# Kernel optimization log

Measured on AMD Instinct MI355X. Metric: run time of the kernel, lower is better.

## Reference

```python
import jax, jax.numpy as jnp
import numpy as np

N, D0, D1, HID, OUT = 4096, 256, 128, 64, 16
R, M, K, PROJ = 3, 2, 2, 128  # meta-path rels, same-type rels, schema rels, attn hidden


def setup_inputs() -> dict:
    key = jax.random.key(0)
    ks = jax.random.split(key, 24)
    g = lambda i, shape, s: jax.random.normal(ks[i], shape, jnp.float32) * s
    return {
        "features0": g(0, (N, D0), 1.0),
        "features1": g(1, (N, D1), 1.0),
        # row-scale adjacencies so aggregated features stay O(1)
        "adj_same": jax.random.uniform(ks[2], (M, N, N), jnp.float32) / N,
        "adj_meta": jax.random.uniform(ks[3], (R, N, N), jnp.float32) / N,
        "adj_schema": jax.random.uniform(ks[4], (K, N, N), jnp.float32) / N,
        "Wm0": g(5, (D0, HID), D0 ** -0.5), "bm0": jnp.zeros((HID,), jnp.float32),
        "Wm1": g(6, (D1, HID), D1 ** -0.5), "bm1": jnp.zeros((HID,), jnp.float32),
        "Wa": g(7, (HID, PROJ), HID ** -0.5), "ba": jnp.zeros((PROJ,), jnp.float32),
        "qa": g(8, (PROJ,), PROJ ** -0.5),
        "ws": g(9, (HID, 1), HID ** -0.5),
        "Wc1": g(10, (HID, PROJ), HID ** -0.5), "bc1": jnp.zeros((PROJ,), jnp.float32),
        "wc2": g(11, (PROJ, 1), PROJ ** -0.5),
        "Wt1": g(12, (HID, PROJ), HID ** -0.5), "bt1": jnp.zeros((PROJ,), jnp.float32),
        "wt2": g(13, (PROJ, 1), PROJ ** -0.5),
        "Wp": g(14, (HID, OUT), HID ** -0.5), "bp": jnp.zeros((OUT,), jnp.float32),
    }


def reference(features0, features1, adj_same, adj_meta, adj_schema,
              Wm0, bm0, Wm1, bm1, Wa, ba, qa, ws, Wc1, bc1, wc2,
              Wt1, bt1, wt2, Wp, bp):
    # per-type feature mapping: tanh(Linear(x))
    h0 = jnp.tanh(features0 @ Wm0 + bm0)  # [N, HID]
    h1 = jnp.tanh(features1 @ Wm1 + bm1)  # [N, HID]

    # --- Dif_Classes_AGG: meta-path aggregation + semantic attention over R relations ---
    hr = jnp.tanh(jnp.einsum('rij,jd->rid', adj_meta, h0))        # [R, N, HID]
    s = jnp.mean(jnp.tanh(hr @ Wa + ba) @ qa, axis=1)             # [R]
    beta_r = jax.nn.softmax(s)                                    # [R]
    relation_agg = jnp.einsum('r,rnd->nd', beta_r, hr)            # [N, HID]

    # --- Weight_Schema: schema-matrix aggregation with per-node softmax over K ---
    zk = jnp.einsum('kij,jd->kid', adj_schema, h1)                # [K, N, HID]
    beta_k = jax.nn.softmax(jnp.squeeze(zk @ ws, -1), axis=0)     # [K, N]
    item_classes_agg = jnp.einsum('kn,knd->nd', beta_k, zk)       # [N, HID]

    # --- Classes_Relation_AGG: same-type (item-item) aggregation over M relations ---
    ym = jnp.tanh(jnp.einsum('mij,jd->mid', adj_same, item_classes_agg))  # [M, N, HID]
    wm = jnp.squeeze(jnp.tanh(ym @ Wc1 + bc1) @ wc2, -1)          # [M, N]
    beta_m = jax.nn.softmax(wm, axis=0)                           # [M, N]
    item_item = jnp.einsum('mn,mnd->nd', beta_m, ym)              # [N, HID]

    # --- AggAttention over the two module outputs ---
    Hs = jnp.stack([relation_agg, item_item], axis=1)             # [N, 2, HID]
    wt = jnp.squeeze(jnp.tanh(Hs @ Wt1 + bt1) @ wt2, -1)          # [N, 2]
    beta_t = jax.nn.softmax(wt, axis=1)[..., None]                # [N, 2, 1]
    H = jnp.sum(beta_t * Hs, axis=1)                              # [N, HID]

    return (H @ Wp + bp, H)
```

## Files before the change

### kernel.cpp

```cpp
#include <hip/hip_runtime.h>

#define NODES 4096

typedef float f32x4 __attribute__((ext_vector_type(4)));
typedef float f32x8 __attribute__((ext_vector_type(8)));
typedef __bf16 bf16x8 __attribute__((ext_vector_type(8)));
typedef unsigned short u16x8 __attribute__((ext_vector_type(8)));

__device__ __forceinline__ unsigned short f2bf(float x) {
    unsigned u = __builtin_bit_cast(unsigned, x);
    return (unsigned short)((u + 0x7fffu + ((u >> 16) & 1u)) >> 16);
}

__device__ __forceinline__ void glds16(const void* g, void* l) {
    __builtin_amdgcn_global_load_lds(
        (const __attribute__((address_space(1))) unsigned int*)g,
        (__attribute__((address_space(3))) unsigned int*)l,
        16, 0, 0);
}

__global__ __launch_bounds__(256) void prep_h(
    const float* __restrict__ f0, const float* __restrict__ f1,
    const float* __restrict__ Wm0, const float* __restrict__ bm0,
    const float* __restrict__ Wm1, const float* __restrict__ bm1,
    unsigned short* __restrict__ hT0, unsigned short* __restrict__ hT1)
{
    const int d = threadIdx.x & 63;
    int n = blockIdx.x * 4 + (threadIdx.x >> 6);
    n = __builtin_amdgcn_readfirstlane(n);
    const float* r0 = f0 + (size_t)n * 256;
    float a0 = bm0[d];
#pragma unroll 8
    for (int k = 0; k < 256; ++k) a0 = fmaf(r0[k], Wm0[k * 64 + d], a0);
    hT0[(size_t)d * NODES + n] = f2bf(tanhf(a0));
    const float* r1 = f1 + (size_t)n * 128;
    float a1 = bm1[d];
#pragma unroll 8
    for (int k = 0; k < 128; ++k) a1 = fmaf(r1[k], Wm1[k * 64 + d], a1);
    hT1[(size_t)d * NODES + n] = f2bf(tanhf(a1));
}

__global__ __launch_bounds__(256, 2) void adj_gemm(
    const float* __restrict__ A0, const float* __restrict__ A1,
    const float* __restrict__ A2, const float* __restrict__ A3,
    const float* __restrict__ A4,
    const unsigned short* __restrict__ hTa, const unsigned short* __restrict__ hTb,
    int split, float* __restrict__ outBase, unsigned tanhMask,
    int khBits, int klen)
{
    __shared__ unsigned short sB[2][64][256];

    const int job = blockIdx.y;
    const float* adj = job == 0 ? A0 : job == 1 ? A1 : job == 2 ? A2 : job == 3 ? A3 : A4;
    const unsigned short* hT = (job < split) ? hTa : hTb;
    const bool doTanh = (tanhMask >> job) & 1u;

    const int bx = blockIdx.x;
    const int group = bx >> khBits;
    const int kh = bx & ((1 << khBits) - 1);
    const int kc0 = kh * klen;
    const int nchunks = klen >> 8;
    const int n0 = group * 64;

    const int lane = threadIdx.x & 63;
    const int wid = threadIdx.x >> 6;
    const int fr = lane & 15, fg = lane >> 4;

    const char* hB = (const char*)hT;
    char* ldsBase = (char*)&sB[0][0][0];

    const int gd_half = lane >> 5;
    const int gd_kb = (lane & 31) * 16;

    const char* aPtr = (const char*)adj +
        ((size_t)(n0 + wid * 16 + fr) * NODES + kc0 + fg * 8) * 4;

    f32x4 acc0 = {0.f,0.f,0.f,0.f}, acc1 = {0.f,0.f,0.f,0.f};
    f32x4 acc2 = {0.f,0.f,0.f,0.f}, acc3 = {0.f,0.f,0.f,0.f};

    {
        const size_t cbyte = (size_t)kc0 * 2;
#pragma unroll
        for (int i = 0; i < 8; ++i) {
            const int seg = wid * 8 + i;
            char* ldst = ldsBase + seg * 1024;
            const int d = seg * 2 + gd_half;
            const int sb = gd_kb ^ ((d & 7) << 4);
            glds16(hB + (size_t)d * (NODES * 2) + cbyte + sb, ldst);
        }
    }
    __syncthreads();

    int cur = 0;
    for (int c = 0; c < nchunks; ++c) {
        if (c + 1 < nchunks) {
            const size_t cbyte = (size_t)(kc0 + ((c + 1) << 8)) * 2;
            const int bufoff = (cur ^ 1) * 32768;
#pragma unroll
            for (int i = 0; i < 8; ++i) {
                const int seg = wid * 8 + i;
                char* ldst = ldsBase + bufoff + seg * 1024;
                const int d = seg * 2 + gd_half;
                const int sb = gd_kb ^ ((d & 7) << 4);
                glds16(hB + (size_t)d * (NODES * 2) + cbyte + sb, ldst);
            }
        }
        const char* bb = ldsBase + cur * 32768;
        const char* aC = aPtr + ((size_t)c << 10);
#pragma unroll
        for (int ks = 0; ks < 8; ++ks) {
            f32x8 av = *(const f32x8*)(aC + (ks << 7));
            bf16x8 af = __builtin_convertvector(av, bf16x8);
            {
                const int dcol = 0 * 16 + fr;
                const int off = dcol * 512 + (((ks << 6) + (fg << 4)) ^ ((dcol & 7) << 4));
                u16x8 bf = *(const u16x8*)(bb + off);
                acc0 = __builtin_amdgcn_mfma_f32_16x16x32_bf16(af, __builtin_bit_cast(bf16x8, bf), acc0, 0, 0, 0);
            }
            {
                const int dcol = 1 * 16 + fr;
                const int off = dcol * 512 + (((ks << 6) + (fg << 4)) ^ ((dcol & 7) << 4));
                u16x8 bf = *(const u16x8*)(bb + off);
                acc1 = __builtin_amdgcn_mfma_f32_16x16x32_bf16(af, __builtin_bit_cast(bf16x8, bf), acc1, 0, 0, 0);
            }
            {
                const int dcol = 2 * 16 + fr;
                const int off = dcol * 512 + (((ks << 6) + (fg << 4)) ^ ((dcol & 7) << 4));
                u16x8 bf = *(const u16x8*)(bb + off);
                acc2 = __builtin_amdgcn_mfma_f32_16x16x32_bf16(af, __builtin_bit_cast(bf16x8, bf), acc2, 0, 0, 0);
            }
            {
                const int dcol = 3 * 16 + fr;
                const int off = dcol * 512 + (((ks << 6) + (fg << 4)) ^ ((dcol & 7) << 4));
                u16x8 bf = *(const u16x8*)(bb + off);
                acc3 = __builtin_amdgcn_mfma_f32_16x16x32_bf16(af, __builtin_bit_cast(bf16x8, bf), acc3, 0, 0, 0);
            }
        }
        __syncthreads();
        cur ^= 1;
    }

    float* outC = outBase + (size_t)((job << khBits) | kh) * (NODES * 64);
    float* Cw = outC + (size_t)(n0 + wid * 16 + fg * 4) * 64 + fr;
#pragma unroll
    for (int j = 0; j < 4; ++j) {
        float v0 = acc0[j], v1 = acc1[j], v2 = acc2[j], v3 = acc3[j];
        if (doTanh) { v0 = tanhf(v0); v1 = tanhf(v1); v2 = tanhf(v2); v3 = tanhf(v3); }
        Cw[(size_t)j * 64 + 0]  = v0; Cw[(size_t)j * 64 + 16] = v1;
        Cw[(size_t)j * 64 + 32] = v2; Cw[(size_t)j * 64 + 48] = v3;
    }
}

__global__ __launch_bounds__(128) void stage_c(
    const float* __restrict__ agg, const float* __restrict__ Wa,
    const float* __restrict__ ba, const float* __restrict__ qa,
    const float* __restrict__ wsv, float* __restrict__ sacc,
    unsigned short* __restrict__ iccT)
{
    const int n = blockIdx.x;
    const int p = threadIdx.x;
    __shared__ float rs[3][2];
    __shared__ float ru[2][2];

    const float* h0p = agg + (size_t)n * 64;
    const float* h1p = agg + ((size_t)NODES + n) * 64;
    const float* h2p = agg + ((size_t)2 * NODES + n) * 64;
    float a0 = ba[p], a1 = a0, a2 = a0;
#pragma unroll 8
    for (int d = 0; d < 64; ++d) {
        float w = Wa[d * 128 + p];
        a0 = fmaf(h0p[d], w, a0);
        a1 = fmaf(h1p[d], w, a1);
        a2 = fmaf(h2p[d], w, a2);
    }
    float qv = qa[p];
    float v0 = tanhf(a0) * qv, v1 = tanhf(a1) * qv, v2 = tanhf(a2) * qv;

    const float* z0 = agg + ((size_t)3 * NODES + n) * 64;
    const float* z1 = agg + ((size_t)4 * NODES + n) * 64;
    float u0 = (p < 64) ? z0[p] * wsv[p] : 0.f;
    float u1 = (p < 64) ? z1[p] * wsv[p] : 0.f;

#pragma unroll
    for (int off = 32; off; off >>= 1) {
        v0 += __shfl_down(v0, off); v1 += __shfl_down(v1, off); v2 += __shfl_down(v2, off);
        u0 += __shfl_down(u0, off); u1 += __shfl_down(u1, off);
    }
    if ((p & 63) == 0) {
        int w = p >> 6;
        rs[0][w] = v0; rs[1][w] = v1; rs[2][w] = v2;
        ru[0][w] = u0; ru[1][w] = u1;
    }
    __syncthreads();
    if (p < 3) atomicAdd(&sacc[p], rs[p][0] + rs[p][1]);

    float U0 = ru[0][0] + ru[0][1];
    float U1 = ru[1][0] + ru[1][1];
    float mx = fmaxf(U0, U1);
    float e0 = expf(U0 - mx), e1 = expf(U1 - mx);
    float inv = 1.f / (e0 + e1);
    if (p < 64) {
        float icc = (e0 * z0[p] + e1 * z1[p]) * inv;
        iccT[(size_t)p * NODES + n] = f2bf(icc);
    }
}

__global__ __launch_bounds__(256) void finalize(
    const float* __restrict__ agg, const float* __restrict__ ymp,
    const float* __restrict__ sacc,
    const float* __restrict__ Wc1, const float* __restrict__ bc1, const float* __restrict__ wc2,
    const float* __restrict__ Wt1, const float* __restrict__ bt1, const float* __restrict__ wt2,
    const float* __restrict__ Wp, const float* __restrict__ bp,
    float* __restrict__ out)
{
    __shared__ float sWc[64 * 128];
    __shared__ float sWp[64 * 16];
    __shared__ float sY0[2][64], sY1[2][64];
    __shared__ float sHs0[2][64], sHs1[2][64], sHv[2][64];
    __shared__ float rA[2][2], rB[2][2];

    const int t = threadIdx.x;
    for (int i = t; i < 64 * 128; i += 256) sWc[i] = Wc1[i];
    for (int i = t; i < 64 * 16; i += 256) sWp[i] = Wp[i];

    float s0 = sacc[0] * (1.f / NODES), s1 = sacc[1] * (1.f / NODES), s2 = sacc[2] * (1.f / NODES);
    float sm = fmaxf(s0, fmaxf(s1, s2));
    float b0 = expf(s0 - sm), b1 = expf(s1 - sm), b2 = expf(s2 - sm);
    float bi = 1.f / (b0 + b1 + b2);
    b0 *= bi; b1 *= bi; b2 *= bi;

    const int sub = t >> 7;
    const int p = t & 127;
    const int wiH = p >> 6;
    const float bcv = bc1[p], wcv = wc2[p], btv = bt1[p], wtv = wt2[p];
    __syncthreads();

    for (int it = 0; it < 8; ++it) {
        const int n = blockIdx.x * 16 + it * 2 + sub;
        if (p < 64) {
            const size_t NN64 = (size_t)NODES * 64;
            float ya = ymp[(size_t)n * 64 + p]            + ymp[NN64 + (size_t)n * 64 + p];
            float yb = ymp[2 * NN64 + (size_t)n * 64 + p] + ymp[3 * NN64 + (size_t)n * 64 + p];
            sY0[sub][p] = tanhf(ya);
            sY1[sub][p] = tanhf(yb);
            sHs0[sub][p] = b0 * agg[(size_t)n * 64 + p]
                         + b1 * agg[((size_t)NODES + n) * 64 + p]
                         + b2 * agg[((size_t)2 * NODES + n) * 64 + p];
        }
        __syncthreads();
        float ac0 = bcv, ac1 = bcv;
#pragma unroll 8
        for (int d = 0; d < 64; ++d) {
            float w = sWc[d * 128 + p];
            ac0 = fmaf(sY0[sub][d], w, ac0);
            ac1 = fmaf(sY1[sub][d], w, ac1);
        }
        float v0 = tanhf(ac0) * wcv, v1 = tanhf(ac1) * wcv;
#pragma unroll
        for (int off = 32; off; off >>= 1) { v0 += __shfl_down(v0, off); v1 += __shfl_down(v1, off); }
        if ((p & 63) == 0) { rA[sub][wiH] = v0; rB[sub][wiH] = v1; }
        __syncthreads();
        float wm0 = rA[sub][0] + rA[sub][1];
        float wm1 = rB[sub][0] + rB[sub][1];
        float mm = fmaxf(wm0, wm1);
        float g0 = expf(wm0 - mm), g1 = expf(wm1 - mm);
        float gi = 1.f / (g0 + g1);
        g0 *= gi; g1 *= gi;
        if (p < 64) sHs1[sub][p] = g0 * sY0[sub][p] + g1 * sY1[sub][p];
        __syncthreads();

        float at0 = btv, at1 = btv;
#pragma unroll 8
        for (int d = 0; d < 64; ++d) {
            float w = Wt1[d * 128 + p];
            at0 = fmaf(sHs0[sub][d], w, at0);
            at1 = fmaf(sHs1[sub][d], w, at1);
        }
        float q0 = tanhf(at0) * wtv, q1 = tanhf(at1) * wtv;
#pragma unroll
        for (int off = 32; off; off >>= 1) { q0 += __shfl_down(q0, off); q1 += __shfl_down(q1, off); }
        if ((p & 63) == 0) { rA[sub][wiH] = q0; rB[sub][wiH] = q1; }
        __syncthreads();
        float t0 = rA[sub][0] + rA[sub][1];
        float t1 = rB[sub][0] + rB[sub][1];
        float tm = fmaxf(t0, t1);
        float c0 = expf(t0 - tm), c1 = expf(t1 - tm);
        float ci = 1.f / (c0 + c1);
        c0 *= ci; c1 *= ci;
        if (p < 64) {
            float H = c0 * sHs0[sub][p] + c1 * sHs1[sub][p];
            sHv[sub][p] = H;
            out[(size_t)NODES * 16 + (size_t)n * 64 + p] = H;
        }
        __syncthreads();
        if (p < 16) {
            float a = bp[p];
#pragma unroll 8
            for (int d = 0; d < 64; ++d) a = fmaf(sHv[sub][d], sWp[d * 16 + p], a);
            out[(size_t)n * 16 + p] = a;
        }
        __syncthreads();
    }
}

extern "C" void kernel_launch(void* const* d_in, const int* in_sizes, int n_in,
                              void* d_out, int out_size, void* d_ws, size_t ws_size,
                              hipStream_t stream)
{
    const float* f0   = (const float*)d_in[0];
    const float* f1   = (const float*)d_in[1];
    const float* adjS = (const float*)d_in[2];
    const float* adjM = (const float*)d_in[3];
    const float* adjK = (const float*)d_in[4];
    const float* Wm0  = (const float*)d_in[5];
    const float* bm0  = (const float*)d_in[6];
    const float* Wm1  = (const float*)d_in[7];
    const float* bm1  = (const float*)d_in[8];
    const float* Wa   = (const float*)d_in[9];
    const float* ba   = (const float*)d_in[10];
    const float* qa   = (const float*)d_in[11];
    const float* wsv  = (const float*)d_in[12];
    const float* Wc1  = (const float*)d_in[13];
    const float* bc1  = (const float*)d_in[14];
    const float* wc2  = (const float*)d_in[15];
    const float* Wt1  = (const float*)d_in[16];
    const float* bt1  = (const float*)d_in[17];
    const float* wt2  = (const float*)d_in[18];
    const float* Wp   = (const float*)d_in[19];
    const float* bpv  = (const float*)d_in[20];
    float* out = (float*)d_out;

    char* ws = (char*)d_ws;
    unsigned short* hT0  = (unsigned short*)(ws);
    unsigned short* hT1  = (unsigned short*)(ws + 524288);
    unsigned short* iccT = (unsigned short*)(ws + 1048576);
    float* agg           = (float*)(ws + 1572864);
    float* ymp           = (float*)(ws + 4718592);
    float* sacc          = (float*)(ws + 8912896);

    hipMemsetAsync(sacc, 0, 64, stream);
    prep_h<<<dim3(1024), dim3(256), 0, stream>>>(f0, f1, Wm0, bm0, Wm1, bm1, hT0, hT1);

    const size_t NNs = (size_t)NODES * NODES;
    adj_gemm<<<dim3(64, 5), dim3(256), 0, stream>>>(
        adjM, adjM + NNs, adjM + 2 * NNs, adjK, adjK + NNs,
        hT0, hT1, 3, agg, 0x7u, 0, 4096);
    stage_c<<<dim3(4096), dim3(128), 0, stream>>>(agg, Wa, ba, qa, wsv, sacc, iccT);
    adj_gemm<<<dim3(128, 2), dim3(256), 0, stream>>>(
        adjS, adjS + NNs, adjS, adjS, adjS,
        iccT, iccT, 5, ymp, 0x0u, 1, 2048);
    finalize<<<dim3(256), dim3(256), 0, stream>>>(
        agg, ymp, sacc, Wc1, bc1, wc2, Wt1, bt1, wt2, Wp, bpv, out);
}
```

Baseline: 299.1 us.

## Stream adjacency tiles through LDS with async loads alongside bf16 h tiles

The adjacency GEMM previously read fp32 adjacency rows directly from global memory into registers while only the h operand was staged in LDS. Now both the adjacency tile and the h tile are fetched with global_load_lds into a double-buffered 96KB LDS region using XOR swizzles. Prefetch runs two chunks ahead, with explicit vmcnt waits and raw barriers. The chunk size is halved to 128 columns and the occupancy hint is dropped. The aim is to hide HBM latency of the dominant fp32 adjacency stream, at the cost of more LDS (likely one block per CU) and hand-tuned waitcnt correctness.

Measured after the change: 256.1 us. 1.17x faster.

```diff
diff --git a/kernel.cpp b/kernel.cpp
--- a/kernel.cpp
+++ b/kernel.cpp
@@ -40,7 +40,7 @@
     hT1[(size_t)d * NODES + n] = f2bf(tanhf(a1));
 }
 
-__global__ __launch_bounds__(256, 2) void adj_gemm(
+__global__ __launch_bounds__(256) void adj_gemm(
     const float* __restrict__ A0, const float* __restrict__ A1,
     const float* __restrict__ A2, const float* __restrict__ A3,
     const float* __restrict__ A4,
@@ -48,7 +48,7 @@
     int split, float* __restrict__ outBase, unsigned tanhMask,
     int khBits, int klen)
 {
-    __shared__ unsigned short sB[2][64][256];
+    __shared__ __align__(16) char smem[2 * 49152];
 
     const int job = blockIdx.y;
     const float* adj = job == 0 ? A0 : job == 1 ? A1 : job == 2 ? A2 : job == 3 ? A3 : A4;
@@ -59,86 +59,101 @@
     const int group = bx >> khBits;
     const int kh = bx & ((1 << khBits) - 1);
     const int kc0 = kh * klen;
-    const int nchunks = klen >> 8;
+    const int nc = klen >> 7;
     const int n0 = group * 64;
 
     const int lane = threadIdx.x & 63;
     const int wid = threadIdx.x >> 6;
     const int fr = lane & 15, fg = lane >> 4;
 
-    const char* hB = (const char*)hT;
-    char* ldsBase = (char*)&sB[0][0][0];
-
-    const int gd_half = lane >> 5;
-    const int gd_kb = (lane & 31) * 16;
-
-    const char* aPtr = (const char*)adj +
-        ((size_t)(n0 + wid * 16 + fr) * NODES + kc0 + fg * 8) * 4;
+    const char* aBase = (const char*)adj;
+    const char* hBase = (const char*)hT;
+    const char* aSrc[8]; int aDst[8];
+#pragma unroll
+    for (int i = 0; i < 8; ++i) {
+        const int seg = wid * 8 + i;
+        const int rowc = seg * 2 + (lane >> 5);
+        const int kbs = (lane & 31) * 16;
+        const int kb = kbs ^ ((rowc & 7) << 4);
+        aSrc[i] = aBase + (size_t)(n0 + rowc) * (NODES * 4) + (size_t)kc0 * 4 + kb;
+        aDst[i] = seg * 1024;
+    }
+    const char* bSrc[4]; int bDst[4];
+#pragma unroll
+    for (int i = 0; i < 4; ++i) {
+        const int seg = wid * 4 + i;
+        const int d = seg * 4 + (lane >> 4);
+        const int kbs = (lane & 15) * 16;
+        const int kb = kbs ^ ((d & 7) << 4);
+        bSrc[i] = hBase + (size_t)d * (NODES * 2) + (size_t)kc0 * 2 + kb;
+        bDst[i] = 32768 + seg * 1024;
+    }
+
+#define STAGE(c)                                                          \
+    {                                                                     \
+        char* dstb = smem + ((c) & 1) * 49152;                            \
+        const size_t aoff = (size_t)(c) * 512;                            \
+        const size_t boff = (size_t)(c) * 256;                            \
+        _Pragma("unroll")                                                 \
+        for (int i = 0; i < 8; ++i) glds16(aSrc[i] + aoff, dstb + aDst[i]); \
+        _Pragma("unroll")                                                 \
+        for (int i = 0; i < 4; ++i) glds16(bSrc[i] + boff, dstb + bDst[i]); \
+    }
 
     f32x4 acc0 = {0.f,0.f,0.f,0.f}, acc1 = {0.f,0.f,0.f,0.f};
     f32x4 acc2 = {0.f,0.f,0.f,0.f}, acc3 = {0.f,0.f,0.f,0.f};
 
-    {
-        const size_t cbyte = (size_t)kc0 * 2;
-#pragma unroll
-        for (int i = 0; i < 8; ++i) {
-            const int seg = wid * 8 + i;
-            char* ldst = ldsBase + seg * 1024;
-            const int d = seg * 2 + gd_half;
-            const int sb = gd_kb ^ ((d & 7) << 4);
-            glds16(hB + (size_t)d * (NODES * 2) + cbyte + sb, ldst);
-        }
-    }
-    __syncthreads();
-
-    int cur = 0;
-    for (int c = 0; c < nchunks; ++c) {
-        if (c + 1 < nchunks) {
-            const size_t cbyte = (size_t)(kc0 + ((c + 1) << 8)) * 2;
-            const int bufoff = (cur ^ 1) * 32768;
-#pragma unroll
-            for (int i = 0; i < 8; ++i) {
-                const int seg = wid * 8 + i;
-                char* ldst = ldsBase + bufoff + seg * 1024;
-                const int d = seg * 2 + gd_half;
-                const int sb = gd_kb ^ ((d & 7) << 4);
-                glds16(hB + (size_t)d * (NODES * 2) + cbyte + sb, ldst);
-            }
-        }
-        const char* bb = ldsBase + cur * 32768;
-        const char* aC = aPtr + ((size_t)c << 10);
-#pragma unroll
-        for (int ks = 0; ks < 8; ++ks) {
-            f32x8 av = *(const f32x8*)(aC + (ks << 7));
+    const int rowA = wid * 16 + fr;
+    const int swzA = (rowA & 7) << 4;
+
+    STAGE(0);
+    STAGE(1);
+
+    for (int c = 0; c < nc; ++c) {
+        if (c + 1 < nc) { asm volatile("s_waitcnt vmcnt(12)" ::: "memory"); }
+        else            { asm volatile("s_waitcnt vmcnt(0)"  ::: "memory"); }
+        __builtin_amdgcn_sched_barrier(0);
+        __builtin_amdgcn_s_barrier();
+        __builtin_amdgcn_sched_barrier(0);
+
+        const char* bb = smem + (c & 1) * 49152;
+        const char* aRow = bb + rowA * 512;
+#pragma unroll
+        for (int ks = 0; ks < 4; ++ks) {
+            const int kb = ks * 128 + fg * 32;
+            f32x4 alo = *(const f32x4*)(aRow + ((kb)      ^ swzA));
+            f32x4 ahi = *(const f32x4*)(aRow + ((kb + 16) ^ swzA));
+            f32x8 av = __builtin_shufflevector(alo, ahi, 0,1,2,3,4,5,6,7);
             bf16x8 af = __builtin_convertvector(av, bf16x8);
+            const int kb2 = ks * 64 + fg * 16;
             {
                 const int dcol = 0 * 16 + fr;
-                const int off = dcol * 512 + (((ks << 6) + (fg << 4)) ^ ((dcol & 7) << 4));
-                u16x8 bf = *(const u16x8*)(bb + off);
-                acc0 = __builtin_amdgcn_mfma_f32_16x16x32_bf16(af, __builtin_bit_cast(bf16x8, bf), acc0, 0, 0, 0);
+                u16x8 bv = *(const u16x8*)(bb + 32768 + dcol * 256 + (kb2 ^ ((dcol & 7) << 4)));
+                acc0 = __builtin_amdgcn_mfma_f32_16x16x32_bf16(af, __builtin_bit_cast(bf16x8, bv), acc0, 0, 0, 0);
             }
             {
                 const int dcol = 1 * 16 + fr;
-                const int off = dcol * 512 + (((ks << 6) + (fg << 4)) ^ ((dcol & 7) << 4));
-                u16x8 bf = *(const u16x8*)(bb + off);
-                acc1 = __builtin_amdgcn_mfma_f32_16x16x32_bf16(af, __builtin_bit_cast(bf16x8, bf), acc1, 0, 0, 0);
+                u16x8 bv = *(const u16x8*)(bb + 32768 + dcol * 256 + (kb2 ^ ((dcol & 7) << 4)));
+                acc1 = __builtin_amdgcn_mfma_f32_16x16x32_bf16(af, __builtin_bit_cast(bf16x8, bv), acc1, 0, 0, 0);
             }
             {
                 const int dcol = 2 * 16 + fr;
-                const int off = dcol * 512 + (((ks << 6) + (fg << 4)) ^ ((dcol & 7) << 4));
-                u16x8 bf = *(const u16x8*)(bb + off);
-                acc2 = __builtin_amdgcn_mfma_f32_16x16x32_bf16(af, __builtin_bit_cast(bf16x8, bf), acc2, 0, 0, 0);
+                u16x8 bv = *(const u16x8*)(bb + 32768 + dcol * 256 + (kb2 ^ ((dcol & 7) << 4)));
+                acc2 = __builtin_amdgcn_mfma_f32_16x16x32_bf16(af, __builtin_bit_cast(bf16x8, bv), acc2, 0, 0, 0);
             }
             {
                 const int dcol = 3 * 16 + fr;
-                const int off = dcol * 512 + (((ks << 6) + (fg << 4)) ^ ((dcol & 7) << 4));
-                u16x8 bf = *(const u16x8*)(bb + off);
-                acc3 = __builtin_amdgcn_mfma_f32_16x16x32_bf16(af, __builtin_bit_cast(bf16x8, bf), acc3, 0, 0, 0);
+                u16x8 bv = *(const u16x8*)(bb + 32768 + dcol * 256 + (kb2 ^ ((dcol & 7) << 4)));
+                acc3 = __builtin_amdgcn_mfma_f32_16x16x32_bf16(af, __builtin_bit_cast(bf16x8, bv), acc3, 0, 0, 0);
             }
         }
-        __syncthreads();
-        cur ^= 1;
-    }
+
+        __builtin_amdgcn_sched_barrier(0);
+        __builtin_amdgcn_s_barrier();
+        __builtin_amdgcn_sched_barrier(0);
+        if (c + 2 < nc) STAGE(c + 2);
+    }
+#undef STAGE
 
     float* outC = outBase + (size_t)((job << khBits) | kh) * (NODES * 64);
     float* Cw = outC + (size_t)(n0 + wid * 16 + fg * 4) * 64 + fr;
```
